# Kernel tuning notes

Hardware: AMD Instinct MI355X
Metric: run time of the kernel (lower is better)

## Reference

```python
import jax, jax.numpy as jnp
import numpy as np

FILTER_SIZE = 3  # from init_kwargs


def setup_inputs() -> dict:
    key = jax.random.key(0)
    k1, k2 = jax.random.split(key)
    B, C, H, W = 4, 3, 384, 1248
    left_input = jax.random.uniform(k1, (B, C, H, W), dtype=jnp.float32)
    right_input = jax.random.uniform(k2, (B, C, H, W), dtype=jnp.float32)
    return {"left_input": left_input, "right_input": right_input}


def _extract_patches(x, f):
    # Faithful to conv3d with one-hot (identity) filters of kernel (1,f,f),
    # padding (0, f//2, f//2): out[b, k*C+c, y, x] = x_padded[b, c, y+dy, x+dx]
    B, C, H, W = x.shape
    pad = f // 2
    xp = jnp.pad(x, ((0, 0), (0, 0), (pad, pad), (pad, pad)))
    # [B, f*f, C, H, W]: shift index k = dy*f + dx (row-major over kernel window)
    patches = jnp.stack(
        [xp[:, :, dy:dy + H, dx:dx + W] for dy in range(f) for dx in range(f)],
        axis=1,
    )
    return patches.reshape(B, f * f * C, H, W)


def reference(left_input, right_input):
    f = FILTER_SIZE
    left_features = _extract_patches(left_input, f)
    right_features = _extract_patches(right_input, f)
    # one_hot_filter[k, 0, 0, i, j] = 1 iff i*f + j == k (identity unfold filter)
    one_hot_filter = jnp.eye(f * f, dtype=jnp.float32).reshape(f * f, 1, 1, f, f)
    return (left_features, right_features, one_hot_filter)
```

## Files before the change

### kernel.cpp

```cpp
#include <hip/hip_runtime.h>

#define B_ 4
#define C_ 3
#define H_ 384
#define W_ 1248
#define F_ 3
#define KK_ 9
#define W4_ (W_ / 4)

constexpr int N_FEAT = B_ * KK_ * C_ * H_ * W_;
constexpr int NTH    = B_ * C_ * H_ * W4_;

typedef float vf4 __attribute__((ext_vector_type(4)));

__global__ __launch_bounds__(256) void unfold9_kernel(
    const float* __restrict__ left,
    const float* __restrict__ right,
    float* __restrict__ out)
{
    int t = blockIdx.x * blockDim.x + threadIdx.x;
    if (t >= NTH) return;

    int x4 = t % W4_;
    int r  = t / W4_;
    int y  = r % H_;
    int r2 = r / H_;
    int c  = r2 % C_;
    int b  = r2 / C_;
    int x0 = x4 * 4;

    const size_t inbase = ((size_t)(b * C_ + c)) * H_ * W_;
    const float* ins[2] = { left, right };

    vf4   m[2][3];
    float lf[2][3], rg[2][3];

    #pragma unroll
    for (int s = 0; s < 2; ++s) {
        #pragma unroll
        for (int dy = 0; dy < 3; ++dy) {
            int yin = y + dy - 1;
            if (yin >= 0 && yin < H_) {
                const float* rp = ins[s] + inbase + (size_t)yin * W_;
                m[s][dy]  = *reinterpret_cast<const vf4*>(rp + x0);
                lf[s][dy] = (x0 > 0)        ? rp[x0 - 1] : 0.f;
                rg[s][dy] = (x0 + 4 < W_)   ? rp[x0 + 4] : 0.f;
            } else {
                m[s][dy]  = (vf4){0.f, 0.f, 0.f, 0.f};
                lf[s][dy] = 0.f;
                rg[s][dy] = 0.f;
            }
        }
    }

    const size_t row_off = (((size_t)(b * KK_) * C_ + c) * H_ + y) * W_ + x0;
    const size_t kstride = (size_t)C_ * H_ * W_;

    #pragma unroll
    for (int s = 0; s < 2; ++s) {
        float* ob = out + (size_t)s * N_FEAT + row_off;
        #pragma unroll
        for (int dy = 0; dy < 3; ++dy) {
            vf4 mm = m[s][dy];
            vf4 vL = (vf4){lf[s][dy], mm.x, mm.y, mm.z};
            vf4 vR = (vf4){mm.y, mm.z, mm.w, rg[s][dy]};
            __builtin_nontemporal_store(
                vL, reinterpret_cast<vf4*>(ob + (size_t)(dy * 3 + 0) * kstride));
            __builtin_nontemporal_store(
                mm, reinterpret_cast<vf4*>(ob + (size_t)(dy * 3 + 1) * kstride));
            __builtin_nontemporal_store(
                vR, reinterpret_cast<vf4*>(ob + (size_t)(dy * 3 + 2) * kstride));
        }
    }
}

__global__ void onehot_kernel(float* __restrict__ out)
{
    int i = threadIdx.x;
    if (i < KK_ * KK_) out[i] = (i % 10 == 0) ? 1.0f : 0.0f;
}

extern "C" void kernel_launch(void* const* d_in, const int* in_sizes, int n_in,
                              void* d_out, int out_size, void* d_ws, size_t ws_size,
                              hipStream_t stream)
{
    const float* left  = (const float*)d_in[0];
    const float* right = (const float*)d_in[1];
    float* out = (float*)d_out;

    int blocks = (NTH + 255) / 256;
    unfold9_kernel<<<blocks, 256, 0, stream>>>(left, right, out);
    onehot_kernel<<<1, 128, 0, stream>>>(out + (size_t)2 * N_FEAT);
}
```

Before: 442.3 us.

## Map one thread per output vector for fully linear coalesced stores

Changes the thread mapping from one thread per input float4 (which wrote 18 scattered output vectors) to one thread per output float4, indexed linearly over the whole output. Each thread decodes its shift index and loads one possibly unaligned float4 from the input row, so stores become perfectly contiguous across the grid. The trade-off is 18x more threads and repeated input reads, which are served mostly from cache, plus misaligned vector loads for the shifted taps.

```diff
diff --git a/kernel.cpp b/kernel.cpp
--- a/kernel.cpp
+++ b/kernel.cpp
@@ -9,69 +9,54 @@
 #define W4_ (W_ / 4)
 
 constexpr int N_FEAT = B_ * KK_ * C_ * H_ * W_;
-constexpr int NTH    = B_ * C_ * H_ * W4_;
+constexpr int NTOT4  = 2 * B_ * KK_ * C_ * H_ * W4_;
 
 typedef float vf4 __attribute__((ext_vector_type(4)));
 
-__global__ __launch_bounds__(256) void unfold9_kernel(
+__global__ __launch_bounds__(256) void unfold9_lin(
     const float* __restrict__ left,
     const float* __restrict__ right,
     float* __restrict__ out)
 {
     int t = blockIdx.x * blockDim.x + threadIdx.x;
-    if (t >= NTH) return;
+    if (t >= NTOT4) return;
 
     int x4 = t % W4_;
     int r  = t / W4_;
-    int y  = r % H_;
-    int r2 = r / H_;
-    int c  = r2 % C_;
-    int b  = r2 / C_;
-    int x0 = x4 * 4;
+    int y  = r % H_;  r /= H_;
+    int c  = r % C_;  r /= C_;
+    int k  = r % KK_; r /= KK_;
+    int b  = r % B_;
+    int s  = r / B_;
 
-    const size_t inbase = ((size_t)(b * C_ + c)) * H_ * W_;
-    const float* ins[2] = { left, right };
+    const int dy  = k / 3;
+    const int dx  = k % 3;
+    const int yin = y + dy - 1;
 
-    vf4   m[2][3];
-    float lf[2][3], rg[2][3];
-
-    #pragma unroll
-    for (int s = 0; s < 2; ++s) {
-        #pragma unroll
-        for (int dy = 0; dy < 3; ++dy) {
-            int yin = y + dy - 1;
-            if (yin >= 0 && yin < H_) {
-                const float* rp = ins[s] + inbase + (size_t)yin * W_;
-                m[s][dy]  = *reinterpret_cast<const vf4*>(rp + x0);
-                lf[s][dy] = (x0 > 0)        ? rp[x0 - 1] : 0.f;
-                rg[s][dy] = (x0 + 4 < W_)   ? rp[x0 + 4] : 0.f;
+    vf4 v = (vf4){0.f, 0.f, 0.f, 0.f};
+    if (yin >= 0 && yin < H_) {
+        const float* rp = (s ? right : left)
+                        + (size_t)((b * C_ + c) * H_ + yin) * W_;
+        const int x0 = x4 * 4;
+        if (dx == 1) {
+            v = *reinterpret_cast<const vf4*>(rp + x0);
+        } else if (dx == 0) {
+            if (x4 > 0) {
+                v = *reinterpret_cast<const vf4*>(rp + x0 - 1);
             } else {
-                m[s][dy]  = (vf4){0.f, 0.f, 0.f, 0.f};
-                lf[s][dy] = 0.f;
-                rg[s][dy] = 0.f;
+                vf4 a = *reinterpret_cast<const vf4*>(rp);
+                v = (vf4){0.f, a.x, a.y, a.z};
+            }
+        } else {
+            if (x4 < W4_ - 1) {
+                v = *reinterpret_cast<const vf4*>(rp + x0 + 1);
+            } else {
+                vf4 a = *reinterpret_cast<const vf4*>(rp + x0);
+                v = (vf4){a.y, a.z, a.w, 0.f};
             }
         }
     }
-
-    const size_t row_off = (((size_t)(b * KK_) * C_ + c) * H_ + y) * W_ + x0;
-    const size_t kstride = (size_t)C_ * H_ * W_;
-
-    #pragma unroll
-    for (int s = 0; s < 2; ++s) {
-        float* ob = out + (size_t)s * N_FEAT + row_off;
-        #pragma unroll
-        for (int dy = 0; dy < 3; ++dy) {
-            vf4 mm = m[s][dy];
-            vf4 vL = (vf4){lf[s][dy], mm.x, mm.y, mm.z};
-            vf4 vR = (vf4){mm.y, mm.z, mm.w, rg[s][dy]};
-            __builtin_nontemporal_store(
-                vL, reinterpret_cast<vf4*>(ob + (size_t)(dy * 3 + 0) * kstride));
-            __builtin_nontemporal_store(
-                mm, reinterpret_cast<vf4*>(ob + (size_t)(dy * 3 + 1) * kstride));
-            __builtin_nontemporal_store(
-                vR, reinterpret_cast<vf4*>(ob + (size_t)(dy * 3 + 2) * kstride));
-        }
-    }
+    __builtin_nontemporal_store(v, reinterpret_cast<vf4*>(out) + t);
 }
 
 __global__ void onehot_kernel(float* __restrict__ out)
@@ -88,7 +73,7 @@
     const float* right = (const float*)d_in[1];
     float* out = (float*)d_out;
 
-    int blocks = (NTH + 255) / 256;
-    unfold9_kernel<<<blocks, 256, 0, stream>>>(left, right, out);
+    int blocks = (NTOT4 + 255) / 256;
+    unfold9_lin<<<blocks, 256, 0, stream>>>(left, right, out);
     onehot_kernel<<<1, 128, 0, stream>>>(out + (size_t)2 * N_FEAT);
 }
```

New measurement: 450.7 us. No clear change (+1.9%).
